# Optimization experiments

Measured on AMD Instinct MI355X. Metric: run time of the kernel, lower is better.

The kernel has to match this reference:

```python
import jax, jax.numpy as jnp
import numpy as np

N_EMBD = 1024
N_HEAD = 16
HEAD_DIM = N_EMBD // N_HEAD
D_FF = 4 * N_EMBD


def dyt(x, alpha, gamma, beta):
    # Dynamic Tanh normalizer: gamma * tanh(alpha * x) + beta
    return gamma * jnp.tanh(x * alpha) + beta


def setup_inputs() -> dict:
    key = jax.random.key(0)
    ks = jax.random.split(key, 9)
    C, F = N_EMBD, D_FF
    s = 0.02
    return {
        "x": jax.random.normal(ks[0], (2, 2048, C), dtype=jnp.float32),
        "alpha": jnp.ones((1,), jnp.float32) * 0.5,
        "gamma": jnp.ones((C,), jnp.float32),
        "beta": jnp.zeros((C,), jnp.float32),
        "w_attn": jax.random.normal(ks[1], (C, 3 * C), jnp.float32) * s,
        "b_attn": jnp.zeros((3 * C,), jnp.float32),
        "w_proj": jax.random.normal(ks[2], (C, C), jnp.float32) * s,
        "b_proj": jnp.zeros((C,), jnp.float32),
        "w_fc": jax.random.normal(ks[3], (C, F), jnp.float32) * s,
        "b_fc": jnp.zeros((F,), jnp.float32),
        "w_fc2": jax.random.normal(ks[4], (F, C), jnp.float32) * s,
        "b_fc2": jnp.zeros((C,), jnp.float32),
    }


def reference(x, alpha, gamma, beta, w_attn, b_attn, w_proj, b_proj,
              w_fc, b_fc, w_fc2, b_fc2):
    B, T, C = x.shape
    H, D = N_HEAD, HEAD_DIM

    # --- attention branch (pre-norm with DyT) ---
    h = dyt(x, alpha, gamma, beta)
    qkv = h @ w_attn + b_attn                      # [B,T,3C]
    q, k, v = jnp.split(qkv, 3, axis=-1)
    q = q.reshape(B, T, H, D).transpose(0, 2, 1, 3)  # [B,H,T,D]
    k = k.reshape(B, T, H, D).transpose(0, 2, 1, 3)
    v = v.reshape(B, T, H, D).transpose(0, 2, 1, 3)

    scores = jnp.einsum('bhqd,bhkd->bhqk', q, k) / jnp.sqrt(jnp.asarray(D, x.dtype))
    causal = jnp.tril(jnp.ones((T, T), bool))
    scores = jnp.where(causal[None, None], scores, -jnp.inf)
    attn = jax.nn.softmax(scores, axis=-1)          # [B,H,T,T]
    out = jnp.einsum('bhqk,bhkd->bhqd', attn, v)    # [B,H,T,D]
    out = out.transpose(0, 2, 1, 3).reshape(B, T, C)
    x = x + (out @ w_proj + b_proj)

    # --- MLP branch (pre-norm with same DyT params, as in source) ---
    h2 = dyt(x, alpha, gamma, beta)
    mlp = jax.nn.gelu(h2 @ w_fc + b_fc, approximate=False) @ w_fc2 + b_fc2
    return x + mlp
```

## Files before the change

### kernel.cpp

```cpp
#include <hip/hip_runtime.h>
#include <cstdint>
#include <cstddef>

typedef __bf16 bf16;
typedef __bf16 bf16x8 __attribute__((ext_vector_type(8)));
typedef __bf16 bf16x4 __attribute__((ext_vector_type(4)));
typedef float f32x4 __attribute__((ext_vector_type(4)));

#define DEVI __device__ __forceinline__

DEVI void gload_lds16(const bf16* g, bf16* l) {
    __builtin_amdgcn_global_load_lds(
        (const __attribute__((address_space(1))) void*)(const void*)g,
        (__attribute__((address_space(3))) void*)(void*)l, 16, 0, 0);
}

DEVI float fast_tanh(float y) {
    float t = __builtin_amdgcn_exp2f(2.88539008f * y);
    return 1.f - 2.f * __builtin_amdgcn_rcpf(1.f + t);
}

__global__ void conv_t_kernel(const float* __restrict__ W, bf16* __restrict__ Wt,
                              int K, int N) {
    __shared__ float tile[64][65];
    const int tid = threadIdx.x;
    const int c  = tid & 63;
    const int r4 = tid >> 6;
    const int n0 = blockIdx.x * 64;
    const int k0 = blockIdx.y * 64;
#pragma unroll
    for (int r = 0; r < 64; r += 4)
        tile[r + r4][c] = W[(size_t)(k0 + r + r4) * N + n0 + c];
    __syncthreads();
#pragma unroll
    for (int r = 0; r < 64; r += 4)
        Wt[(size_t)(n0 + r + r4) * K + k0 + c] = (bf16)tile[c][r + r4];
}

__global__ void dyt_kernel(const float* __restrict__ x, const float* __restrict__ alpha,
                           const float* __restrict__ gamma, const float* __restrict__ beta,
                           bf16* __restrict__ h, int total) {
    int i4 = (blockIdx.x * 256 + threadIdx.x) * 4;
    if (i4 >= total) return;
    float a = alpha[0];
    float4 xv = *(const float4*)&x[i4];
    int c = i4 & 1023;
    float4 g  = *(const float4*)&gamma[c];
    float4 bt = *(const float4*)&beta[c];
    bf16x4 o;
    o[0] = (bf16)(g.x * fast_tanh(xv.x * a) + bt.x);
    o[1] = (bf16)(g.y * fast_tanh(xv.y * a) + bt.y);
    o[2] = (bf16)(g.z * fast_tanh(xv.z * a) + bt.z);
    o[3] = (bf16)(g.w * fast_tanh(xv.w * a) + bt.w);
    *(bf16x4*)&h[i4] = o;
}

__global__ void reduce2_kernel(const float* __restrict__ p, const float* __restrict__ bias,
                               const float* __restrict__ resid, float* __restrict__ out,
                               int total) {
    int i4 = (blockIdx.x * 256 + threadIdx.x) * 4;
    if (i4 >= total) return;
    float4 a = *(const float4*)&p[i4];
    float4 bsec = *(const float4*)&p[(size_t)total + i4];
    float4 r = *(const float4*)&resid[i4];
    int c = i4 & 1023;
    float4 bb = *(const float4*)&bias[c];
    float4 o;
    o.x = a.x + bsec.x + r.x + bb.x;
    o.y = a.y + bsec.y + r.y + bb.y;
    o.z = a.z + bsec.z + r.z + bb.z;
    o.w = a.w + bsec.w + r.w + bb.w;
    *(float4*)&out[i4] = o;
}

__global__ void reduce2_dyt_kernel(const float* __restrict__ p, const float* __restrict__ bias,
                                   const float* __restrict__ resid,
                                   float* __restrict__ xout, bf16* __restrict__ hout,
                                   const float* __restrict__ alpha,
                                   const float* __restrict__ gamma,
                                   const float* __restrict__ beta, int total) {
    int i4 = (blockIdx.x * 256 + threadIdx.x) * 4;
    if (i4 >= total) return;
    float a = alpha[0];
    float4 p0 = *(const float4*)&p[i4];
    float4 p1 = *(const float4*)&p[(size_t)total + i4];
    float4 r  = *(const float4*)&resid[i4];
    int c = i4 & 1023;
    float4 bb = *(const float4*)&bias[c];
    float4 g  = *(const float4*)&gamma[c];
    float4 bt = *(const float4*)&beta[c];
    float4 v;
    v.x = p0.x + p1.x + r.x + bb.x;
    v.y = p0.y + p1.y + r.y + bb.y;
    v.z = p0.z + p1.z + r.z + bb.z;
    v.w = p0.w + p1.w + r.w + bb.w;
    *(float4*)&xout[i4] = v;
    bf16x4 o;
    o[0] = (bf16)(g.x * fast_tanh(v.x * a) + bt.x);
    o[1] = (bf16)(g.y * fast_tanh(v.y * a) + bt.y);
    o[2] = (bf16)(g.z * fast_tanh(v.z * a) + bt.z);
    o[3] = (bf16)(g.w * fast_tanh(v.w * a) + bt.w);
    *(bf16x4*)&hout[i4] = o;
}

template<int OP>
__global__ void gemm_kernel(const bf16* __restrict__ A, const bf16* __restrict__ Wt,
                            const float* __restrict__ bias, const float* resid,
                            float* outf, bf16* outb,
                            const float* __restrict__ alpha_p,
                            const float* __restrict__ gamma,
                            const float* __restrict__ beta,
                            int M, int N, int K, int lda, int ldb) {
    __shared__ bf16 As[2][128 * 32];
    __shared__ bf16 Bs[2][128 * 32];
    const int tid  = threadIdx.x;
    const int lane = tid & 63;
    const int w    = tid >> 6;
    const int wr   = w >> 1, wc = w & 1;

    const int nwgx = gridDim.x;
    const int nwg  = gridDim.x * gridDim.y;
    const int orig = blockIdx.y * nwgx + blockIdx.x;
    const int cpx  = nwg >> 3;
    const int swz  = (orig & 7) * cpx + (orig >> 3);
    const int bm = (swz / nwgx) * 128;
    const int bn = (swz % nwgx) * 128;
    const int kz = blockIdx.z * K;

    f32x4 acc[4][4] = {};

    const int srow = tid >> 2;
    const int sgrp = ((tid & 3) ^ ((srow >> 1) & 3)) * 8;
    const bf16* a0 = A  + (size_t)(bm + srow) * lda + kz + sgrp;
    const bf16* a1 = a0 + (size_t)64 * lda;
    const bf16* b0 = Wt + (size_t)(bn + srow) * ldb + kz + sgrp;
    const bf16* b1 = b0 + (size_t)64 * ldb;

    auto stage = [&](int buf) {
        gload_lds16(a0, &As[buf][tid * 8]);
        gload_lds16(a1, &As[buf][2048 + tid * 8]);
        gload_lds16(b0, &Bs[buf][tid * 8]);
        gload_lds16(b1, &Bs[buf][2048 + tid * 8]);
        a0 += 32; a1 += 32; b0 += 32; b1 += 32;
    };

    const int lh = lane >> 4, lm = lane & 15;
    const int arow = wr * 64 + lm;
    const int brow = wc * 64 + lm;
    const int gsw = (lh ^ ((lm >> 1) & 3)) * 8;

    stage(0);
    __syncthreads();

    const int nk = K >> 5;
    for (int kt = 0; kt < nk; ++kt) {
        const int cur = kt & 1;
        if (kt + 1 < nk) stage(cur ^ 1);
        bf16x8 af[4], bfr[4];
#pragma unroll
        for (int i = 0; i < 4; i++)
            af[i] = *(const bf16x8*)&As[cur][(arow + i * 16) * 32 + gsw];
#pragma unroll
        for (int i = 0; i < 4; i++)
            bfr[i] = *(const bf16x8*)&Bs[cur][(brow + i * 16) * 32 + gsw];
#pragma unroll
        for (int i = 0; i < 4; i++)
#pragma unroll
            for (int j = 0; j < 4; j++)
                acc[i][j] = __builtin_amdgcn_mfma_f32_16x16x32_bf16(af[i], bfr[j], acc[i][j], 0, 0, 0);
        __syncthreads();
    }

#pragma unroll
    for (int i = 0; i < 4; i++) {
        const int row0 = bm + wr * 64 + i * 16 + lh * 4;
#pragma unroll
        for (int jf = 0; jf < 4; jf++) {
            const int col = bn + wc * 64 + jf * 16 + lm;
            const float bval = (OP == 4) ? 0.f : bias[col];
#pragma unroll
            for (int r = 0; r < 4; r++) {
                const int row = row0 + r;
                const size_t idx = (size_t)row * N + col;
                float v = acc[i][jf][r] + bval;
                if (OP == 0) {
                    const float qs = (col < 1024) ? 0.18033688011f : 1.0f;
                    outb[idx] = (bf16)(v * qs);
                } else if (OP == 1) {
                    v += resid[idx];
                    outf[idx] = v;
                    float hh = gamma[col] * fast_tanh(v * alpha_p[0]) + beta[col];
                    outb[idx] = (bf16)hh;
                } else if (OP == 2) {
                    float xc = v * (1.f + 0.044715f * v * v);
                    float g = v * __builtin_amdgcn_rcpf(
                        1.f + __builtin_amdgcn_exp2f(-2.30220795f * xc));
                    outb[idx] = (bf16)g;
                } else if (OP == 3) {
                    v += resid[idx];
                    outf[idx] = v;
                } else {
                    outf[(size_t)blockIdx.z * M * N + idx] = v;
                }
            }
        }
    }
}

__global__ void __launch_bounds__(256, 2)
attn_kernel(const bf16* __restrict__ qkv, bf16* __restrict__ out) {
    const int j  = blockIdx.x;
    const int bh = blockIdx.y;
    const int b = bh >> 4, h = bh & 15;
    const int tid = threadIdx.x, lane = tid & 63, w = tid >> 6;
    const int T = 2048;
    const size_t C3 = 3072;
    const bf16* qb = qkv + (size_t)b * T * C3 + h * 64;
    const bf16* kb = qb + 1024;
    const bf16* vb = qb + 2048;

    __shared__ bf16 Ks[2][64][64];
    __shared__ bf16 Vt[2][64][72];
    __shared__ bf16 Pl[2][4][16][72];

    const int tA = j, tB = 31 - j;
    const int qA = tA * 64 + w * 16;
    const int qB = tB * 64 + w * 16;
    const int lm = lane & 15;
    const int lh = lane >> 4;

    bf16x8 qfA0, qfA1, qfB0, qfB1;
    {
        size_t qo = (size_t)(qA + lm) * C3 + lh * 8;
        qfA0 = *(const bf16x8*)&qb[qo];
        qfA1 = *(const bf16x8*)&qb[qo + 32];
        qo = (size_t)(qB + lm) * C3 + lh * 8;
        qfB0 = *(const bf16x8*)&qb[qo];
        qfB1 = *(const bf16x8*)&qb[qo + 32];
    }
    f32x4 accA[4] = {}, accB[4] = {};
    float mA = -1e30f, lA = 0.f, mB = -1e30f, lB = 0.f;

    const int nt = tB + 1;
    const int sg = tid & 7;
    const int sq = tid >> 3;
    bf16x8 rv[4];

    const int krow = tid >> 3;
    const int kcb  = tid & 7;
    const int kcbs = (kcb ^ (krow & 7)) * 8;
    auto stageK = [&](int buf, int k0) {
        gload_lds16(&kb[(size_t)(k0 + krow) * C3 + kcbs],      &Ks[buf][0][0]  + tid * 8);
        gload_lds16(&kb[(size_t)(k0 + 32 + krow) * C3 + kcbs], &Ks[buf][32][0] + tid * 8);
    };
    auto loadV = [&](int k0) {
        if (tid < 128) {
#pragma unroll
            for (int i = 0; i < 4; ++i)
                rv[i] = *(const bf16x8*)&vb[(size_t)(k0 + sq * 4 + i) * C3 + sg * 8];
        }
    };
    auto writeV = [&](int buf) {
        if (tid < 128) {
            const int cbase = ((((sq >> 1) ^ sg) & 7) << 3) + ((sq & 1) << 2);
#pragma unroll
            for (int e = 0; e < 8; ++e) {
                bf16x4 wv;
                wv[0] = rv[0][e]; wv[1] = rv[1][e]; wv[2] = rv[2][e]; wv[3] = rv[3][e];
                *(bf16x4*)&Vt[buf][sg * 8 + e][cbase] = wv;
            }
        }
    };

    auto softmax_pv = [&](f32x4 (&s)[4], f32x4 (&acc)[4], float& mS, float& lS,
                          int qg, bool diag, int k0, int slot, bf16x8 (&vf)[2][4]) {
        if (diag) {
#pragma unroll
            for (int f = 0; f < 4; ++f)
#pragma unroll
                for (int r = 0; r < 4; ++r) {
                    const int kgl = k0 + f * 16 + lh * 4 + r;
                    s[f][r] = (kgl > qg) ? -1e30f : s[f][r];
                }
        }
        float a0 = fmaxf(fmaxf(s[0][0], s[0][1]), s[0][2]);
        float a1 = fmaxf(fmaxf(s[0][3], s[1][0]), s[1][1]);
        float a2 = fmaxf(fmaxf(s[1][2], s[1][3]), s[2][0]);
        float a3 = fmaxf(fmaxf(s[2][1], s[2][2]), s[2][3]);
        float a4 = fmaxf(fmaxf(s[3][0], s[3][1]), s[3][2]);
        float b0 = fmaxf(fmaxf(a0, a1), a2);
        float b1 = fmaxf(fmaxf(a3, a4), s[3][3]);
        float pm = fmaxf(b0, b1);
        pm = fmaxf(pm, __shfl_xor(pm, 16));
        pm = fmaxf(pm, __shfl_xor(pm, 32));
        if (!__all(pm - mS <= 8.f)) {
            const float mnew = fmaxf(mS, pm);
            const float corr = __builtin_amdgcn_exp2f(mS - mnew);
            mS = mnew;
            lS *= corr;
#pragma unroll
            for (int df = 0; df < 4; ++df)
#pragma unroll
                for (int r = 0; r < 4; ++r) acc[df][r] *= corr;
        }
        float rs = 0.f;
#pragma unroll
        for (int f = 0; f < 4; ++f) {
            bf16x4 pw;
#pragma unroll
            for (int r = 0; r < 4; ++r) {
                const float pv = __builtin_amdgcn_exp2f(s[f][r] - mS);
                rs += pv;
                pw[r] = (bf16)pv;
            }
            *(bf16x4*)&Pl[slot][w][lm][f * 16 + lh * 4] = pw;
        }
        rs += __shfl_xor(rs, 16);
        rs += __shfl_xor(rs, 32);
        lS += rs;
        __builtin_amdgcn_s_setprio(1);
#pragma unroll
        for (int kk = 0; kk < 2; ++kk) {
            bf16x8 pa = *(const bf16x8*)&Pl[slot][w][lm][kk * 32 + lh * 8];
#pragma unroll
            for (int df = 0; df < 4; ++df)
                acc[df] = __builtin_amdgcn_mfma_f32_16x16x32_bf16(vf[kk][df], pa, acc[df], 0, 0, 0);
        }
        __builtin_amdgcn_s_setprio(0);
    };

    stageK(0, 0);
    loadV(0);
    writeV(0);
    __syncthreads();

    for (int kt = 0; kt < nt; ++kt) {
        const int k0 = kt * 64;
        const int buf = kt & 1;
        const bool hasNext = (kt + 1 < nt);
        if (hasNext) {
            stageK(buf ^ 1, k0 + 64);
            loadV(k0 + 64);
        }

        bf16x8 kf[4][2];
#pragma unroll
        for (int f = 0; f < 4; ++f) {
            const int row = f * 16 + lm;
            const int sw = (row & 7);
            kf[f][0] = *(const bf16x8*)&Ks[buf][row][(lh ^ sw) * 8];
            kf[f][1] = *(const bf16x8*)&Ks[buf][row][((lh + 4) ^ sw) * 8];
        }
        bf16x8 vf[2][4];
#pragma unroll
        for (int kk = 0; kk < 2; ++kk)
#pragma unroll
            for (int df = 0; df < 4; ++df) {
                const int dr = df * 16 + lm;
                vf[kk][df] = *(const bf16x8*)&Vt[buf][dr][(((4 * kk + lh) ^ ((dr >> 3) & 7)) << 3)];
            }

        const bool actA = (kt <= tA);
        f32x4 sA[4], sB[4];
        __builtin_amdgcn_s_setprio(1);
#pragma unroll
        for (int f = 0; f < 4; ++f) {
            f32x4 z = {};
            z = __builtin_amdgcn_mfma_f32_16x16x32_bf16(kf[f][0], qfB0, z, 0, 0, 0);
            z = __builtin_amdgcn_mfma_f32_16x16x32_bf16(kf[f][1], qfB1, z, 0, 0, 0);
            sB[f] = z;
        }
        if (actA) {
#pragma unroll
            for (int f = 0; f < 4; ++f) {
                f32x4 z = {};
                z = __builtin_amdgcn_mfma_f32_16x16x32_bf16(kf[f][0], qfA0, z, 0, 0, 0);
                z = __builtin_amdgcn_mfma_f32_16x16x32_bf16(kf[f][1], qfA1, z, 0, 0, 0);
                sA[f] = z;
            }
        }
        __builtin_amdgcn_s_setprio(0);

        if (actA)
            softmax_pv(sA, accA, mA, lA, qA + lm, kt == tA, k0, 0, vf);
        if (hasNext) writeV(buf ^ 1);
        softmax_pv(sB, accB, mB, lB, qB + lm, kt == tB, k0, 1, vf);
        __syncthreads();
    }

    bf16* obase = out + (size_t)b * T * 1024 + h * 64;
    {
        const float linv = 1.0f / lA;
        bf16* ob = obase + (size_t)(qA + lm) * 1024;
#pragma unroll
        for (int df = 0; df < 4; ++df) {
            bf16x4 st;
#pragma unroll
            for (int r = 0; r < 4; ++r) st[r] = (bf16)(accA[df][r] * linv);
            *(bf16x4*)&ob[df * 16 + lh * 4] = st;
        }
    }
    {
        const float linv = 1.0f / lB;
        bf16* ob = obase + (size_t)(qB + lm) * 1024;
#pragma unroll
        for (int df = 0; df < 4; ++df) {
            bf16x4 st;
#pragma unroll
            for (int r = 0; r < 4; ++r) st[r] = (bf16)(accB[df][r] * linv);
            *(bf16x4*)&ob[df * 16 + lh * 4] = st;
        }
    }
}

extern "C" void kernel_launch(void* const* d_in, const int* in_sizes, int n_in,
                              void* d_out, int out_size, void* d_ws, size_t ws_size,
                              hipStream_t stream) {
    const float* x      = (const float*)d_in[0];
    const float* alpha  = (const float*)d_in[1];
    const float* gamma  = (const float*)d_in[2];
    const float* beta   = (const float*)d_in[3];
    const float* w_attn = (const float*)d_in[4];
    const float* b_attn = (const float*)d_in[5];
    const float* w_proj = (const float*)d_in[6];
    const float* b_proj = (const float*)d_in[7];
    const float* w_fc   = (const float*)d_in[8];
    const float* b_fc   = (const float*)d_in[9];
    const float* w_fc2  = (const float*)d_in[10];
    const float* b_fc2  = (const float*)d_in[11];
    float* out = (float*)d_out;

    const int M = 4096, C = 1024, F = 4096;
    char* ws = (char*)d_ws;
    bf16* wt_attn = (bf16*)ws;
    bf16* wt_proj = wt_attn + (size_t)3 * C * C;
    bf16* wt_fc   = wt_proj + (size_t)C * C;
    bf16* wt_fc2  = wt_fc   + (size_t)F * C;
    bf16* hbuf    = wt_fc2  + (size_t)C * F;
    bf16* qkvbuf  = hbuf    + (size_t)M * C;
    bf16* aout    = qkvbuf  + (size_t)M * F;
    float* x2     = (float*)(aout + (size_t)M * C);
    float* part   = x2 + (size_t)M * C;
    const size_t need = (size_t)(88 + 32) * 1024 * 1024;
    const bool splitK = ws_size >= need;

    dim3 blk(256);
    conv_t_kernel<<<dim3(3 * C / 64, C / 64), blk, 0, stream>>>(w_attn, wt_attn, C, 3 * C);
    conv_t_kernel<<<dim3(C / 64, C / 64),     blk, 0, stream>>>(w_proj, wt_proj, C, C);
    conv_t_kernel<<<dim3(F / 64, C / 64),     blk, 0, stream>>>(w_fc,   wt_fc,   C, F);
    conv_t_kernel<<<dim3(C / 64, F / 64),     blk, 0, stream>>>(w_fc2,  wt_fc2,  F, C);

    dyt_kernel<<<dim3(M * C / 1024), blk, 0, stream>>>(x, alpha, gamma, beta, hbuf, M * C);

    gemm_kernel<0><<<dim3(3 * C / 128, M / 128), blk, 0, stream>>>(
        hbuf, wt_attn, b_attn, nullptr, nullptr, qkvbuf, nullptr, nullptr, nullptr,
        M, 3 * C, C, C, C);

    attn_kernel<<<dim3(16, 32), blk, 0, stream>>>(qkvbuf, aout);

    if (splitK) {
        gemm_kernel<4><<<dim3(C / 128, M / 128, 2), blk, 0, stream>>>(
            aout, wt_proj, b_proj, nullptr, part, nullptr, nullptr, nullptr, nullptr,
            M, C, C / 2, C, C);
        reduce2_dyt_kernel<<<dim3(M * C / 1024), blk, 0, stream>>>(
            part, b_proj, x, x2, hbuf, alpha, gamma, beta, M * C);
    } else {
        gemm_kernel<1><<<dim3(C / 128, M / 128), blk, 0, stream>>>(
            aout, wt_proj, b_proj, x, x2, hbuf, alpha, gamma, beta,
            M, C, C, C, C);
    }

    gemm_kernel<2><<<dim3(F / 128, M / 128), blk, 0, stream>>>(
        hbuf, wt_fc, b_fc, nullptr, nullptr, qkvbuf, nullptr, nullptr, nullptr,
        M, F, C, C, C);

    if (splitK) {
        gemm_kernel<4><<<dim3(C / 128, M / 128, 2), blk, 0, stream>>>(
            qkvbuf, wt_fc2, b_fc2, nullptr, part, nullptr, nullptr, nullptr, nullptr,
            M, C, F / 2, F, F);
        reduce2_kernel<<<dim3(M * C / 1024), blk, 0, stream>>>(part, b_fc2, x2, out, M * C);
    } else {
        gemm_kernel<3><<<dim3(C / 128, M / 128), blk, 0, stream>>>(
            qkvbuf, wt_fc2, b_fc2, x2, out, nullptr, nullptr, nullptr, nullptr,
            M, C, F, F, F);
    }
}
```

Before: 240.7 us.

## Use 256x256-tile 512-thread GEMM for MLP layers with 4-way bf16 split-K

Adds a new 256x256 tile GEMM kernel with 512 threads, double-buffered LDS via direct global-to-LDS loads, XOR-swizzled shared layout, workgroup swizzling and setprio around MFMA clusters. It replaces the FC1 (GELU) GEMM and the FC2 split-K GEMM. FC2 now splits K four ways, writes partials in bf16, and reduces them with a new reduce4 kernel. The larger tiles are meant to raise data reuse and MFMA utilisation. In exchange the FC2 grid shrinks to 64x4 blocks, and storing partials in bf16 loses precision.

```diff
diff --git a/kernel.cpp b/kernel.cpp
--- a/kernel.cpp
+++ b/kernel.cpp
@@ -70,6 +70,26 @@
     o.y = a.y + bsec.y + r.y + bb.y;
     o.z = a.z + bsec.z + r.z + bb.z;
     o.w = a.w + bsec.w + r.w + bb.w;
+    *(float4*)&out[i4] = o;
+}
+
+__global__ void reduce4_kernel(const bf16* __restrict__ p, const float* __restrict__ bias,
+                               const float* __restrict__ resid, float* __restrict__ out,
+                               int total) {
+    int i4 = (blockIdx.x * 256 + threadIdx.x) * 4;
+    if (i4 >= total) return;
+    bf16x4 q0 = *(const bf16x4*)&p[i4];
+    bf16x4 q1 = *(const bf16x4*)&p[(size_t)total + i4];
+    bf16x4 q2 = *(const bf16x4*)&p[(size_t)2 * total + i4];
+    bf16x4 q3 = *(const bf16x4*)&p[(size_t)3 * total + i4];
+    float4 r = *(const float4*)&resid[i4];
+    int c = i4 & 1023;
+    float4 bb = *(const float4*)&bias[c];
+    float4 o;
+    o.x = (float)q0[0] + (float)q1[0] + (float)q2[0] + (float)q3[0] + r.x + bb.x;
+    o.y = (float)q0[1] + (float)q1[1] + (float)q2[1] + (float)q3[1] + r.y + bb.y;
+    o.z = (float)q0[2] + (float)q1[2] + (float)q2[2] + (float)q3[2] + r.z + bb.z;
+    o.w = (float)q0[3] + (float)q1[3] + (float)q2[3] + (float)q3[3] + r.w + bb.w;
     *(float4*)&out[i4] = o;
 }
 
@@ -191,16 +211,141 @@
                     outf[idx] = v;
                     float hh = gamma[col] * fast_tanh(v * alpha_p[0]) + beta[col];
                     outb[idx] = (bf16)hh;
-                } else if (OP == 2) {
+                } else if (OP == 3) {
+                    v += resid[idx];
+                    outf[idx] = v;
+                } else if (OP == 4) {
+                    outf[(size_t)blockIdx.z * M * N + idx] = v;
+                }
+            }
+        }
+    }
+}
+
+template<int OP>
+__global__ void __launch_bounds__(512, 2)
+gemm256_kernel(const bf16* __restrict__ A, const bf16* __restrict__ Wt,
+               const float* __restrict__ bias,
+               bf16* __restrict__ outb, bf16* __restrict__ outpb,
+               int M, int N, int K, int lda, int ldb) {
+    __shared__ bf16 As[2][256][64];
+    __shared__ bf16 Bs[2][256][64];
+    const int tid  = threadIdx.x;
+    const int lane = tid & 63;
+    const int w    = tid >> 6;
+    const int wr   = w >> 2;
+    const int wcn  = w & 3;
+    const int lh = lane >> 4, lm = lane & 15;
+
+    const int nwgx = gridDim.x;
+    const int nwg  = gridDim.x * gridDim.y;
+    const int orig = blockIdx.y * nwgx + blockIdx.x;
+    const int cpx  = nwg >> 3;
+    const int swz  = (orig & 7) * cpx + (orig >> 3);
+    const int bm = (swz / nwgx) * 256;
+    const int bn = (swz % nwgx) * 256;
+    const int kz = blockIdx.z * K;
+
+    f32x4 acc[8][4] = {};
+
+    const int srow = tid >> 3;
+    const int sgr  = ((tid & 7) ^ (srow & 7)) * 8;
+    const bf16* aSrc = A  + (size_t)(bm + srow) * lda + kz + sgr;
+    const bf16* bSrc = Wt + (size_t)(bn + srow) * ldb + kz + sgr;
+
+    auto STAGE = [&](int b, int kt) {
+#pragma unroll
+        for (int l = 0; l < 4; ++l)
+            gload_lds16(aSrc + (size_t)(l * 64) * lda + kt * 64,
+                        &As[b][0][0] + (l * 512 + tid) * 8);
+#pragma unroll
+        for (int l = 0; l < 4; ++l)
+            gload_lds16(bSrc + (size_t)(l * 64) * ldb + kt * 64,
+                        &Bs[b][0][0] + (l * 512 + tid) * 8);
+    };
+
+    auto COMPUTE4 = [&](int b) {
+#pragma unroll
+        for (int q = 0; q < 4; ++q) {
+            const int qm = q & 1, qn = q >> 1;
+            bf16x8 af[4][2], bfr[2][2];
+#pragma unroll
+            for (int mf = 0; mf < 4; ++mf) {
+                const int row = wr * 128 + (qm * 4 + mf) * 16 + lm;
+                const int sw = row & 7;
+#pragma unroll
+                for (int ks = 0; ks < 2; ++ks)
+                    af[mf][ks] = *(const bf16x8*)&As[b][row][((ks * 4 + lh) ^ sw) * 8];
+            }
+#pragma unroll
+            for (int nf = 0; nf < 2; ++nf) {
+                const int row = wcn * 64 + (qn * 2 + nf) * 16 + lm;
+                const int sw = row & 7;
+#pragma unroll
+                for (int ks = 0; ks < 2; ++ks)
+                    bfr[nf][ks] = *(const bf16x8*)&Bs[b][row][((ks * 4 + lh) ^ sw) * 8];
+            }
+            __builtin_amdgcn_s_barrier();
+            asm volatile("s_waitcnt lgkmcnt(0)" ::: "memory");
+            __builtin_amdgcn_sched_barrier(0);
+            __builtin_amdgcn_s_setprio(1);
+#pragma unroll
+            for (int mf = 0; mf < 4; ++mf)
+#pragma unroll
+                for (int nf = 0; nf < 2; ++nf)
+#pragma unroll
+                    for (int ks = 0; ks < 2; ++ks)
+                        acc[qm * 4 + mf][qn * 2 + nf] = __builtin_amdgcn_mfma_f32_16x16x32_bf16(
+                            af[mf][ks], bfr[nf][ks], acc[qm * 4 + mf][qn * 2 + nf], 0, 0, 0);
+            __builtin_amdgcn_s_setprio(0);
+            __builtin_amdgcn_s_barrier();
+        }
+    };
+
+    const int nk = K >> 6;
+    STAGE(0, 0);
+    STAGE(1, 1);
+    asm volatile("s_waitcnt vmcnt(8)" ::: "memory");
+    __builtin_amdgcn_s_barrier();
+    __builtin_amdgcn_sched_barrier(0);
+
+    for (int kt = 0; kt < nk; kt += 2) {
+        COMPUTE4(0);
+        if (kt + 2 < nk) {
+            STAGE(0, kt + 2);
+            asm volatile("s_waitcnt vmcnt(8)" ::: "memory");
+        } else {
+            asm volatile("s_waitcnt vmcnt(0)" ::: "memory");
+        }
+        __builtin_amdgcn_s_barrier();
+        __builtin_amdgcn_sched_barrier(0);
+        COMPUTE4(1);
+        if (kt + 3 < nk) {
+            STAGE(1, kt + 3);
+            asm volatile("s_waitcnt vmcnt(8)" ::: "memory");
+            __builtin_amdgcn_s_barrier();
+            __builtin_amdgcn_sched_barrier(0);
+        }
+    }
+
+#pragma unroll
+    for (int mf = 0; mf < 8; ++mf) {
+        const int row0 = bm + wr * 128 + mf * 16 + lh * 4;
+#pragma unroll
+        for (int nf = 0; nf < 4; ++nf) {
+            const int col = bn + wcn * 64 + nf * 16 + lm;
+            const float bval = (OP == 4) ? 0.f : bias[col];
+#pragma unroll
+            for (int r = 0; r < 4; ++r) {
+                const size_t idx = (size_t)(row0 + r) * N + col;
+                float v = acc[mf][nf][r] + bval;
+                if (OP == 2) {
                     float xc = v * (1.f + 0.044715f * v * v);
                     float g = v * __builtin_amdgcn_rcpf(
                         1.f + __builtin_amdgcn_exp2f(-2.30220795f * xc));
                     outb[idx] = (bf16)g;
-                } else if (OP == 3) {
-                    v += resid[idx];
-                    outf[idx] = v;
                 } else {
-                    outf[(size_t)blockIdx.z * M * N + idx] = v;
+                    outpb[(size_t)blockIdx.z * M * N + idx] = (bf16)v;
                 }
             }
         }
@@ -441,6 +586,7 @@
     bf16* aout    = qkvbuf  + (size_t)M * F;
     float* x2     = (float*)(aout + (size_t)M * C);
     float* part   = x2 + (size_t)M * C;
+    bf16* part4   = (bf16*)part;
     const size_t need = (size_t)(88 + 32) * 1024 * 1024;
     const bool splitK = ws_size >= need;
 
@@ -470,15 +616,13 @@
             M, C, C, C, C);
     }
 
-    gemm_kernel<2><<<dim3(F / 128, M / 128), blk, 0, stream>>>(
-        hbuf, wt_fc, b_fc, nullptr, nullptr, qkvbuf, nullptr, nullptr, nullptr,
-        M, F, C, C, C);
+    gemm256_kernel<2><<<dim3(F / 256, M / 256), dim3(512), 0, stream>>>(
+        hbuf, wt_fc, b_fc, qkvbuf, nullptr, M, F, C, C, C);
 
     if (splitK) {
-        gemm_kernel<4><<<dim3(C / 128, M / 128, 2), blk, 0, stream>>>(
-            qkvbuf, wt_fc2, b_fc2, nullptr, part, nullptr, nullptr, nullptr, nullptr,
-            M, C, F / 2, F, F);
-        reduce2_kernel<<<dim3(M * C / 1024), blk, 0, stream>>>(part, b_fc2, x2, out, M * C);
+        gemm256_kernel<4><<<dim3(C / 256, M / 256, 4), dim3(512), 0, stream>>>(
+            qkvbuf, wt_fc2, b_fc2, nullptr, part4, M, C, F / 4, F, F);
+        reduce4_kernel<<<dim3(M * C / 1024), blk, 0, stream>>>(part4, b_fc2, x2, out, M * C);
     } else {
         gemm_kernel<3><<<dim3(C / 128, M / 128), blk, 0, stream>>>(
             qkvbuf, wt_fc2, b_fc2, x2, out, nullptr, nullptr, nullptr, nullptr,
```

Result: no change. 244.6 us (+1.6%).
